# Kernel tuning notes

Hardware: AMD Instinct MI355X
Metric: run time of the kernel (lower is better)

The kernel has to match this reference:

```python
import jax, jax.numpy as jnp
import numpy as np


def setup_inputs() -> dict:
    key = jax.random.key(0)
    ks = jax.random.split(key, 10)
    B, N, E = 8, 20000, 320000
    IN, H = 128, 64
    x = jax.random.normal(ks[0], (B, N, IN), dtype=jnp.float32)
    additional_features = jax.random.normal(ks[1], (B, 1), dtype=jnp.float32)
    edge_index = jax.random.randint(ks[2], (2, E), 0, N, dtype=jnp.int32)
    # GCNConv params (weight applied as x @ W, plus bias)
    W1 = jax.random.normal(ks[3], (IN, H), dtype=jnp.float32) / np.sqrt(IN)
    b1 = jnp.zeros((H,), dtype=jnp.float32)
    W2 = jax.random.normal(ks[4], (H, H), dtype=jnp.float32) / np.sqrt(H)
    b2 = jnp.zeros((H,), dtype=jnp.float32)
    # fc: Linear(hidden + 1, 1)
    fc_w = jax.random.normal(ks[5], (H + 1, 1), dtype=jnp.float32) / np.sqrt(H + 1)
    fc_b = jnp.zeros((1,), dtype=jnp.float32)
    return {"x": x, "additional_features": additional_features, "edge_index": edge_index,
            "W1": W1, "b1": b1, "W2": W2, "b2": b2, "fc_w": fc_w, "fc_b": fc_b}


def reference(x, additional_features, edge_index, W1, b1, W2, b2, fc_w, fc_b):
    # x: [B, N, F]; edge_index: [2, E] shared across the batch (as in the torch code)
    B, N, _ = x.shape
    src = edge_index[0]
    dst = edge_index[1]
    # GCN with self-loops: deg = 1 + in-degree, symmetric normalization
    deg = jnp.ones((N,), jnp.float32).at[dst].add(1.0)
    dis = jax.lax.rsqrt(deg)                      # deg^{-1/2}
    enorm = dis[src] * dis[dst]                   # per-edge norm
    self_norm = (dis * dis)[None, :, None]        # self-loop norm = 1/deg

    def gcn(h, W, b):
        hw = jnp.einsum('bnf,fo->bno', h, W)      # linear transform first
        msgs = hw[:, src, :] * enorm[None, :, None]
        agg = jnp.zeros_like(hw).at[:, dst, :].add(msgs)   # scatter-add to dst
        return agg + hw * self_norm + b

    h = jax.nn.relu(gcn(x, W1, b1))
    h = jax.nn.relu(gcn(h, W2, b2))
    pooled = h.mean(axis=1)                       # global_mean_pool (equal-size graphs)
    cat = jnp.concatenate([pooled, additional_features], axis=1)
    return cat @ fc_w + fc_b                      # [B, 1]
```

## Files before the change

kernel.cpp:

```cpp
#include <hip/hip_runtime.h>

#define BLK 256

typedef __attribute__((ext_vector_type(8))) unsigned short ushort8v;
typedef __attribute__((ext_vector_type(4))) unsigned short ushort4v;
typedef __attribute__((ext_vector_type(8))) short short8v;
typedef __attribute__((ext_vector_type(4))) float f32x4;

static __device__ __forceinline__ float bf2f(unsigned short u) {
    return __uint_as_float(((unsigned)u) << 16);
}
static __device__ __forceinline__ unsigned short f2bf(float f) {
    unsigned u = __float_as_uint(f);
    u += 0x7FFF + ((u >> 16) & 1);
    return (unsigned short)(u >> 16);
}

__global__ void k_init(int* __restrict__ cnt, int N,
                       const float* __restrict__ W1, const float* __restrict__ W2,
                       unsigned short* __restrict__ Wt1, unsigned short* __restrict__ Wt2,
                       int IN, int H) {
    int i = blockIdx.x * BLK + threadIdx.x;
    if (i < N) cnt[i] = 0;
    if (i < IN * H) {
        int k = i / H, c = i % H;
        Wt1[(size_t)c * IN + k] = f2bf(W1[i]);
    }
    if (i < H * H) {
        int k = i / H, c = i % H;
        Wt2[(size_t)c * H + k] = f2bf(W2[i]);
    }
}

__global__ void k_count(const int* __restrict__ dst, int* __restrict__ cnt, int E) {
    int i = blockIdx.x * BLK + threadIdx.x;
    if (i < E) atomicAdd(&cnt[dst[i]], 1);
}

__global__ __launch_bounds__(1024) void k_scan_all(const int* __restrict__ cnt,
                                                   int* __restrict__ rs,
                                                   int* __restrict__ cur, int N) {
    __shared__ int sm[1024];
    const int t = threadIdx.x;
    const int chunk = (N + 1023) >> 10;
    const int lo = t * chunk;
    const int hi = min(lo + chunk, N);
    int s = 0;
    for (int i = lo; i < hi; ++i) s += cnt[i];
    sm[t] = s;
    __syncthreads();
    for (int off = 1; off < 1024; off <<= 1) {
        int v = (t >= off) ? sm[t - off] : 0;
        __syncthreads();
        sm[t] += v;
        __syncthreads();
    }
    int run = sm[t] - s;
    for (int i = lo; i < hi; ++i) {
        int c = cnt[i];
        rs[i] = run; cur[i] = run;
        run += c;
    }
}

__global__ void k_fill(const int* __restrict__ src, const int* __restrict__ dst,
                       const int* __restrict__ cnt, int* __restrict__ cur,
                       int* __restrict__ csrc, float* __restrict__ cw, int E) {
    int e = blockIdx.x * BLK + threadIdx.x;
    if (e >= E) return;
    int d = dst[e], s = src[e];
    int p = atomicAdd(&cur[d], 1);
    csrc[p] = s;
    cw[p] = rsqrtf((1.0f + (float)cnt[s]) * (1.0f + (float)cnt[d]));
}

template <int K>
__global__ __launch_bounds__(BLK) void k_gemm_mfma(const float* __restrict__ A,
                                                   const unsigned short* __restrict__ Wt,
                                                   unsigned short* __restrict__ C,
                                                   int M, int N, int B) {
    constexpr int LDA = K + 8;
    __shared__ unsigned short As[128 * LDA];
    __shared__ unsigned short Bs[64 * LDA];
    const int t = threadIdx.x;
    const int row0 = blockIdx.x * 128;

    for (int i = t; i < 64 * (K / 8); i += BLK) {
        int r = i / (K / 8), c = i % (K / 8);
        *reinterpret_cast<ushort8v*>(&Bs[r * LDA + c * 8]) =
            *reinterpret_cast<const ushort8v*>(Wt + (size_t)r * K + c * 8);
    }
    for (int i = t; i < 128 * (K / 4); i += BLK) {
        int r = i / (K / 4), c = i % (K / 4);
        int gr = row0 + r;
        float4 v = make_float4(0.f, 0.f, 0.f, 0.f);
        if (gr < M) {
            size_t ra = (size_t)(gr % B) * N + (gr / B);
            v = *reinterpret_cast<const float4*>(A + ra * K + c * 4);
        }
        ushort4v o;
        o[0] = f2bf(v.x); o[1] = f2bf(v.y); o[2] = f2bf(v.z); o[3] = f2bf(v.w);
        *reinterpret_cast<ushort4v*>(&As[r * LDA + c * 4]) = o;
    }
    __syncthreads();

    const int w = t >> 6, lane = t & 63;
    const int lrow = lane & 15;
    const int lk = (lane >> 4) * 8;

    f32x4 acc[2][4] = {};
    #pragma unroll
    for (int ks = 0; ks < K / 32; ++ks) {
        short8v a[2], b[4];
        #pragma unroll
        for (int fr = 0; fr < 2; ++fr)
            a[fr] = *reinterpret_cast<const short8v*>(
                &As[(w * 32 + fr * 16 + lrow) * LDA + ks * 32 + lk]);
        #pragma unroll
        for (int fc = 0; fc < 4; ++fc)
            b[fc] = *reinterpret_cast<const short8v*>(
                &Bs[(fc * 16 + lrow) * LDA + ks * 32 + lk]);
        #pragma unroll
        for (int fr = 0; fr < 2; ++fr)
            #pragma unroll
            for (int fc = 0; fc < 4; ++fc)
                acc[fr][fc] = __builtin_amdgcn_mfma_f32_16x16x32_bf16(
                    a[fr], b[fc], acc[fr][fc], 0, 0, 0);
    }

    __syncthreads();
    #pragma unroll
    for (int fr = 0; fr < 2; ++fr)
        #pragma unroll
        for (int fc = 0; fc < 4; ++fc)
            #pragma unroll
            for (int j = 0; j < 4; ++j)
                As[(w * 32 + fr * 16 + (lane >> 4) * 4 + j) * 72 + fc * 16 + lrow] =
                    f2bf(acc[fr][fc][j]);
    __syncthreads();
    for (int i = t; i < 128 * 8; i += BLK) {
        int r = i >> 3, c = i & 7;
        int gr = row0 + r;
        if (gr < M)
            *reinterpret_cast<ushort8v*>(C + (size_t)gr * 64 + c * 8) =
                *reinterpret_cast<const ushort8v*>(&As[r * 72 + c * 8]);
    }
}

#define EDGE_ACC(S, W)                                                              \
    {                                                                               \
        ushort8v _x = *reinterpret_cast<const ushort8v*>(                           \
            hw + (size_t)(S) * 512 + lane * 8);                                     \
        _Pragma("unroll")                                                           \
        for (int j = 0; j < 8; ++j) a[j] = fmaf((W), bf2f(_x[j]), a[j]);            \
    }

__global__ __launch_bounds__(BLK) void k_gather_gemm(const unsigned short* __restrict__ hw,
                                                     const int* __restrict__ rs,
                                                     const int* __restrict__ cnt,
                                                     const int* __restrict__ csrc,
                                                     const float* __restrict__ cw,
                                                     const float* __restrict__ bias,
                                                     const unsigned short* __restrict__ Wt2,
                                                     unsigned short* __restrict__ hw2,
                                                     int N) {
    __shared__ unsigned short Ws[64 * 72];
    __shared__ unsigned short Tile[32 * 72];
    const int t = threadIdx.x;
    const int wv = t >> 6, lane = t & 63;
    const int n = blockIdx.x * 4 + wv;

    for (int i = t; i < 64 * 8; i += BLK) {
        int r = i >> 3, c = i & 7;
        *reinterpret_cast<ushort8v*>(&Ws[r * 72 + c * 8]) =
            *reinterpret_cast<const ushort8v*>(Wt2 + (size_t)r * 64 + c * 8);
    }

    float a[8];
    {
        const int beg = rs[n];
        const int deg = cnt[n];
        const float self = 1.0f / (1.0f + (float)deg);
        const float* bp = bias + (lane & 7) * 8;
        ushort8v v = *reinterpret_cast<const ushort8v*>(hw + (size_t)n * 512 + lane * 8);
        #pragma unroll
        for (int j = 0; j < 8; ++j) a[j] = fmaf(bf2f(v[j]), self, bp[j]);

        int i = 0;
        for (; i + 4 <= deg; i += 4) {
            int s0 = csrc[beg + i],     s1 = csrc[beg + i + 1];
            int s2 = csrc[beg + i + 2], s3 = csrc[beg + i + 3];
            float w0 = cw[beg + i],     w1 = cw[beg + i + 1];
            float w2 = cw[beg + i + 2], w3 = cw[beg + i + 3];
            EDGE_ACC(s0, w0); EDGE_ACC(s1, w1); EDGE_ACC(s2, w2); EDGE_ACC(s3, w3);
        }
        for (; i < deg; ++i) {
            int s0 = csrc[beg + i];
            float w0 = cw[beg + i];
            EDGE_ACC(s0, w0);
        }
    }
    {
        ushort8v o;
        #pragma unroll
        for (int j = 0; j < 8; ++j) o[j] = f2bf(fmaxf(a[j], 0.f));
        *reinterpret_cast<ushort8v*>(&Tile[(wv * 8 + (lane >> 3)) * 72 + (lane & 7) * 8]) = o;
    }
    __syncthreads();

    const int lrow = lane & 15, lk = (lane >> 4) * 8;
    const int r0 = (wv >> 1) * 16, c0 = (wv & 1) * 32;
    f32x4 acc[2] = {};
    #pragma unroll
    for (int ks = 0; ks < 2; ++ks) {
        short8v af = *reinterpret_cast<const short8v*>(&Tile[(r0 + lrow) * 72 + ks * 32 + lk]);
        #pragma unroll
        for (int fc = 0; fc < 2; ++fc) {
            short8v bf_ = *reinterpret_cast<const short8v*>(
                &Ws[(c0 + fc * 16 + lrow) * 72 + ks * 32 + lk]);
            acc[fc] = __builtin_amdgcn_mfma_f32_16x16x32_bf16(af, bf_, acc[fc], 0, 0, 0);
        }
    }
    __syncthreads();
    #pragma unroll
    for (int fc = 0; fc < 2; ++fc)
        #pragma unroll
        for (int j = 0; j < 4; ++j)
            Tile[(r0 + (lane >> 4) * 4 + j) * 72 + c0 + fc * 16 + lrow] = f2bf(acc[fc][j]);
    __syncthreads();
    {
        int r = t >> 3, c = t & 7;
        *reinterpret_cast<ushort8v*>(
            hw2 + (size_t)(blockIdx.x * 4 + (r >> 3)) * 512 + (r & 7) * 64 + c * 8) =
            *reinterpret_cast<const ushort8v*>(&Tile[r * 72 + c * 8]);
    }
}

__global__ __launch_bounds__(BLK) void k_gather_final(const unsigned short* __restrict__ hw,
                                                      const int* __restrict__ rs,
                                                      const int* __restrict__ cnt,
                                                      const int* __restrict__ csrc,
                                                      const float* __restrict__ cw,
                                                      const float* __restrict__ bias,
                                                      const float* __restrict__ fcw,
                                                      float* __restrict__ partial, int N) {
    const int w = threadIdx.x >> 6, lane = threadIdx.x & 63;
    const int n = blockIdx.x * 4 + w;
    float a[8];
    {
        const int beg = rs[n];
        const int deg = cnt[n];
        const float self = 1.0f / (1.0f + (float)deg);
        const float* bp = bias + (lane & 7) * 8;
        ushort8v v = *reinterpret_cast<const ushort8v*>(hw + (size_t)n * 512 + lane * 8);
        #pragma unroll
        for (int j = 0; j < 8; ++j) a[j] = fmaf(bf2f(v[j]), self, bp[j]);

        int i = 0;
        for (; i + 4 <= deg; i += 4) {
            int s0 = csrc[beg + i],     s1 = csrc[beg + i + 1];
            int s2 = csrc[beg + i + 2], s3 = csrc[beg + i + 3];
            float w0 = cw[beg + i],     w1 = cw[beg + i + 1];
            float w2 = cw[beg + i + 2], w3 = cw[beg + i + 3];
            EDGE_ACC(s0, w0); EDGE_ACC(s1, w1); EDGE_ACC(s2, w2); EDGE_ACC(s3, w3);
        }
        for (; i < deg; ++i) {
            int s0 = csrc[beg + i];
            float w0 = cw[beg + i];
            EDGE_ACC(s0, w0);
        }
    }
    __shared__ float sm[4][8];
    const float* fp = fcw + (lane & 7) * 8;
    float s = 0.f;
    #pragma unroll
    for (int j = 0; j < 8; ++j) s = fmaf(fmaxf(a[j], 0.f), fp[j], s);
    #pragma unroll
    for (int off = 1; off < 8; off <<= 1) s += __shfl_xor(s, off, 64);
    if ((lane & 7) == 0) sm[w][lane >> 3] = s;
    __syncthreads();
    if (threadIdx.x < 8)
        partial[(size_t)blockIdx.x * 8 + threadIdx.x] =
            sm[0][threadIdx.x] + sm[1][threadIdx.x] + sm[2][threadIdx.x] + sm[3][threadIdx.x];
}

__global__ void k_finish(const float* __restrict__ partial, int nblk,
                         const float* __restrict__ addf, const float* __restrict__ fcw,
                         const float* __restrict__ fcb, float* __restrict__ out,
                         int N, int H) {
    int b = blockIdx.x;
    float s = 0.f;
    for (int i = threadIdx.x; i < nblk; i += BLK) s += partial[(size_t)i * 8 + b];
    __shared__ float sm[BLK / 64];
    int lane = threadIdx.x & 63, w = threadIdx.x >> 6;
    #pragma unroll
    for (int off = 32; off; off >>= 1) s += __shfl_down(s, off, 64);
    if (lane == 0) sm[w] = s;
    __syncthreads();
    if (threadIdx.x == 0) {
        float t = sm[0] + sm[1] + sm[2] + sm[3];
        out[b] = t / (float)N + addf[b] * fcw[H] + fcb[0];
    }
}

extern "C" void kernel_launch(void* const* d_in, const int* in_sizes, int n_in,
                              void* d_out, int out_size, void* d_ws, size_t ws_size,
                              hipStream_t stream) {
    const float* x    = (const float*)d_in[0];
    const float* addf = (const float*)d_in[1];
    const int*   ei   = (const int*)d_in[2];
    const float* W1   = (const float*)d_in[3];
    const float* b1   = (const float*)d_in[4];
    const float* W2   = (const float*)d_in[5];
    const float* b2   = (const float*)d_in[6];
    const float* fcw  = (const float*)d_in[7];
    const float* fcb  = (const float*)d_in[8];
    float* out = (float*)d_out;

    const int B  = in_sizes[1];
    const int H  = in_sizes[4];
    const int IN = in_sizes[3] / H;
    const int E  = in_sizes[2] / 2;
    const int N  = in_sizes[0] / (B * IN);
    const int* src = ei;
    const int* dst = ei + E;

    const int M = B * N;

    size_t bufsz = (size_t)M * H;
    unsigned short* bufA = (unsigned short*)d_ws;
    unsigned short* bufB = bufA + bufsz;
    int*   cnt   = (int*)(bufB + bufsz);
    int*   rs    = cnt + N;
    int*   cur   = rs + N;
    int*   csrc  = cur + N;
    float* cw    = (float*)(csrc + E);
    unsigned short* Wt1 = (unsigned short*)(cw + E);
    unsigned short* Wt2 = Wt1 + (size_t)H * IN;
    float* partial = (float*)(Wt2 + (size_t)H * H);

    const int nbN = (N + BLK - 1) / BLK;
    const int nbE = (E + BLK - 1) / BLK;
    const int nodes4 = (N + 3) / 4;

    k_init<<<dim3(nbN), dim3(BLK), 0, stream>>>(cnt, N, W1, W2, Wt1, Wt2, IN, H);
    k_count<<<dim3(nbE), dim3(BLK), 0, stream>>>(dst, cnt, E);
    k_scan_all<<<dim3(1), dim3(1024), 0, stream>>>(cnt, rs, cur, N);
    k_fill<<<dim3(nbE), dim3(BLK), 0, stream>>>(src, dst, cnt, cur, csrc, cw, E);

    k_gemm_mfma<128><<<dim3((M + 127) / 128), dim3(BLK), 0, stream>>>(
        x, Wt1, bufA, M, N, B);

    k_gather_gemm<<<dim3(nodes4), dim3(BLK), 0, stream>>>(
        bufA, rs, cnt, csrc, cw, b1, Wt2, bufB, N);

    k_gather_final<<<dim3(nodes4), dim3(BLK), 0, stream>>>(
        bufB, rs, cnt, csrc, cw, b2, fcw, partial, N);

    k_finish<<<dim3(B), dim3(BLK), 0, stream>>>(partial, nodes4, addf, fcw, fcb, out, N, H);
}
```

Measured before the change: 314.4 us.

## Fuse CSR build into cooperative kernel, split node gathers across two waves

The four CSR-building launches are merged into one cooperative kernel that uses grid syncs, with a fallback to the old multi-launch path if the cooperative launch fails. The weight transpose/convert now happens inside each GEMM block instead of in a separate init kernel. Each node's edge gather is split across two wavefronts that take interleaved edges and combine through shared memory, which doubles the waves per node to expose more memory parallelism. The separate final reduction kernel is replaced by atomics plus a last-block-done counter. This trades fewer launches and more latency hiding for redundant per-block weight conversion, a single-block scan inside the cooperative grid, and float atomics with nondeterministic ordering.

Result: slower. 886.5 us (+182.0%).

```diff
diff --git a/kernel.cpp b/kernel.cpp
--- a/kernel.cpp
+++ b/kernel.cpp
@@ -1,4 +1,7 @@
 #include <hip/hip_runtime.h>
+#include <hip/hip_cooperative_groups.h>
+
+namespace cg = cooperative_groups;
 
 #define BLK 256
 
@@ -16,35 +19,75 @@
     return (unsigned short)(u >> 16);
 }
 
-__global__ void k_init(int* __restrict__ cnt, int N,
-                       const float* __restrict__ W1, const float* __restrict__ W2,
-                       unsigned short* __restrict__ Wt1, unsigned short* __restrict__ Wt2,
-                       int IN, int H) {
+__global__ __launch_bounds__(BLK) void k_csr(int* __restrict__ cnt, int* __restrict__ rs,
+                                             int* __restrict__ cur, int* __restrict__ csrc,
+                                             float* __restrict__ cw,
+                                             const int* __restrict__ src,
+                                             const int* __restrict__ dst,
+                                             float* __restrict__ acc, int* __restrict__ ctr,
+                                             int N, int E) {
+    cg::grid_group grid = cg::this_grid();
+    const int t = threadIdx.x;
+    const int gid = blockIdx.x * BLK + t;
+    const int gsz = gridDim.x * BLK;
+
+    for (int i = gid; i < N; i += gsz) cnt[i] = 0;
+    if (gid < 8) acc[gid] = 0.f;
+    if (gid == 8) *ctr = 0;
+    grid.sync();
+
+    for (int i = gid; i < E; i += gsz) atomicAdd(&cnt[dst[i]], 1);
+    grid.sync();
+
+    if (blockIdx.x == 0) {
+        __shared__ int sm[BLK];
+        const int chunk = (N + BLK - 1) / BLK;
+        const int lo = t * chunk, hi = min(lo + chunk, N);
+        int s = 0;
+        for (int i = lo; i < hi; ++i) s += cnt[i];
+        sm[t] = s;
+        __syncthreads();
+        for (int off = 1; off < BLK; off <<= 1) {
+            int v = (t >= off) ? sm[t - off] : 0;
+            __syncthreads();
+            sm[t] += v;
+            __syncthreads();
+        }
+        int run = sm[t] - s;
+        for (int i = lo; i < hi; ++i) {
+            int c = cnt[i];
+            rs[i] = run; cur[i] = run;
+            run += c;
+        }
+    }
+    grid.sync();
+
+    for (int e = gid; e < E; e += gsz) {
+        int d = dst[e], s = src[e];
+        int p = atomicAdd(&cur[d], 1);
+        csrc[p] = s;
+        cw[p] = rsqrtf((1.0f + (float)cnt[s]) * (1.0f + (float)cnt[d]));
+    }
+}
+
+__global__ void k_zero(int* __restrict__ cnt, float* __restrict__ acc,
+                       int* __restrict__ ctr, int N) {
     int i = blockIdx.x * BLK + threadIdx.x;
     if (i < N) cnt[i] = 0;
-    if (i < IN * H) {
-        int k = i / H, c = i % H;
-        Wt1[(size_t)c * IN + k] = f2bf(W1[i]);
-    }
-    if (i < H * H) {
-        int k = i / H, c = i % H;
-        Wt2[(size_t)c * H + k] = f2bf(W2[i]);
-    }
-}
-
+    if (i < 8) acc[i] = 0.f;
+    if (i == 8) *ctr = 0;
+}
 __global__ void k_count(const int* __restrict__ dst, int* __restrict__ cnt, int E) {
     int i = blockIdx.x * BLK + threadIdx.x;
     if (i < E) atomicAdd(&cnt[dst[i]], 1);
 }
-
 __global__ __launch_bounds__(1024) void k_scan_all(const int* __restrict__ cnt,
                                                    int* __restrict__ rs,
                                                    int* __restrict__ cur, int N) {
     __shared__ int sm[1024];
     const int t = threadIdx.x;
     const int chunk = (N + 1023) >> 10;
-    const int lo = t * chunk;
-    const int hi = min(lo + chunk, N);
+    const int lo = t * chunk, hi = min(lo + chunk, N);
     int s = 0;
     for (int i = lo; i < hi; ++i) s += cnt[i];
     sm[t] = s;
@@ -62,7 +105,6 @@
         run += c;
     }
 }
-
 __global__ void k_fill(const int* __restrict__ src, const int* __restrict__ dst,
                        const int* __restrict__ cnt, int* __restrict__ cur,
                        int* __restrict__ csrc, float* __restrict__ cw, int E) {
@@ -76,7 +118,7 @@
 
 template <int K>
 __global__ __launch_bounds__(BLK) void k_gemm_mfma(const float* __restrict__ A,
-                                                   const unsigned short* __restrict__ Wt,
+                                                   const float* __restrict__ W,
                                                    unsigned short* __restrict__ C,
                                                    int M, int N, int B) {
     constexpr int LDA = K + 8;
@@ -85,10 +127,9 @@
     const int t = threadIdx.x;
     const int row0 = blockIdx.x * 128;
 
-    for (int i = t; i < 64 * (K / 8); i += BLK) {
-        int r = i / (K / 8), c = i % (K / 8);
-        *reinterpret_cast<ushort8v*>(&Bs[r * LDA + c * 8]) =
-            *reinterpret_cast<const ushort8v*>(Wt + (size_t)r * K + c * 8);
+    for (int i = t; i < 64 * K; i += BLK) {
+        int k = i >> 6, c = i & 63;
+        Bs[c * LDA + k] = f2bf(W[i]);
     }
     for (int i = t; i < 128 * (K / 4); i += BLK) {
         int r = i / (K / 4), c = i % (K / 4);
@@ -147,12 +188,38 @@
     }
 }
 
-#define EDGE_ACC(S, W)                                                              \
+#define EDGE_ACC(P)                                                                 \
     {                                                                               \
+        int _s = csrc[P];                                                           \
+        float _w = cw[P];                                                           \
         ushort8v _x = *reinterpret_cast<const ushort8v*>(                           \
-            hw + (size_t)(S) * 512 + lane * 8);                                     \
+            hw + (size_t)_s * 512 + lane * 8);                                      \
         _Pragma("unroll")                                                           \
-        for (int j = 0; j < 8; ++j) a[j] = fmaf((W), bf2f(_x[j]), a[j]);            \
+        for (int j = 0; j < 8; ++j) a[j] = fmaf(_w, bf2f(_x[j]), a[j]);             \
+    }
+
+#define GATHER_CORE(NODE)                                                           \
+    float a[8];                                                                     \
+    {                                                                               \
+        const int beg = rs[NODE];                                                   \
+        const int deg = cnt[NODE];                                                  \
+        if (h == 0) {                                                               \
+            const float self = 1.0f / (1.0f + (float)deg);                          \
+            const float* bp = bias + (lane & 7) * 8;                                \
+            ushort8v v = *reinterpret_cast<const ushort8v*>(                        \
+                hw + (size_t)(NODE) * 512 + lane * 8);                              \
+            _Pragma("unroll")                                                       \
+            for (int j = 0; j < 8; ++j) a[j] = fmaf(bf2f(v[j]), self, bp[j]);       \
+        } else {                                                                    \
+            _Pragma("unroll")                                                       \
+            for (int j = 0; j < 8; ++j) a[j] = 0.f;                                 \
+        }                                                                           \
+        int i = beg + h;                                                            \
+        const int end = beg + deg;                                                  \
+        for (; i + 6 < end; i += 8) {                                               \
+            EDGE_ACC(i); EDGE_ACC(i + 2); EDGE_ACC(i + 4); EDGE_ACC(i + 6);         \
+        }                                                                           \
+        for (; i < end; i += 2) EDGE_ACC(i);                                        \
     }
 
 __global__ __launch_bounds__(BLK) void k_gather_gemm(const unsigned short* __restrict__ hw,
@@ -161,77 +228,55 @@
                                                      const int* __restrict__ csrc,
                                                      const float* __restrict__ cw,
                                                      const float* __restrict__ bias,
-                                                     const unsigned short* __restrict__ Wt2,
+                                                     const float* __restrict__ W2,
                                                      unsigned short* __restrict__ hw2,
                                                      int N) {
     __shared__ unsigned short Ws[64 * 72];
-    __shared__ unsigned short Tile[32 * 72];
+    __shared__ unsigned short Tile[16 * 72];
+    __shared__ float comb[2][512];
     const int t = threadIdx.x;
     const int wv = t >> 6, lane = t & 63;
-    const int n = blockIdx.x * 4 + wv;
-
-    for (int i = t; i < 64 * 8; i += BLK) {
-        int r = i >> 3, c = i & 7;
-        *reinterpret_cast<ushort8v*>(&Ws[r * 72 + c * 8]) =
-            *reinterpret_cast<const ushort8v*>(Wt2 + (size_t)r * 64 + c * 8);
-    }
-
-    float a[8];
-    {
-        const int beg = rs[n];
-        const int deg = cnt[n];
-        const float self = 1.0f / (1.0f + (float)deg);
-        const float* bp = bias + (lane & 7) * 8;
-        ushort8v v = *reinterpret_cast<const ushort8v*>(hw + (size_t)n * 512 + lane * 8);
-        #pragma unroll
-        for (int j = 0; j < 8; ++j) a[j] = fmaf(bf2f(v[j]), self, bp[j]);
-
-        int i = 0;
-        for (; i + 4 <= deg; i += 4) {
-            int s0 = csrc[beg + i],     s1 = csrc[beg + i + 1];
-            int s2 = csrc[beg + i + 2], s3 = csrc[beg + i + 3];
-            float w0 = cw[beg + i],     w1 = cw[beg + i + 1];
-            float w2 = cw[beg + i + 2], w3 = cw[beg + i + 3];
-            EDGE_ACC(s0, w0); EDGE_ACC(s1, w1); EDGE_ACC(s2, w2); EDGE_ACC(s3, w3);
-        }
-        for (; i < deg; ++i) {
-            int s0 = csrc[beg + i];
-            float w0 = cw[beg + i];
-            EDGE_ACC(s0, w0);
-        }
-    }
-    {
+    const int s = wv >> 1, h = wv & 1;
+    const int n = blockIdx.x * 2 + s;
+
+    for (int i = t; i < 64 * 64; i += BLK) {
+        int k = i >> 6, c = i & 63;
+        Ws[c * 72 + k] = f2bf(W2[i]);
+    }
+
+    GATHER_CORE(n);
+
+    if (h == 1) {
+        #pragma unroll
+        for (int j = 0; j < 8; ++j) comb[s][j * 64 + lane] = a[j];
+    }
+    __syncthreads();
+    if (h == 0) {
         ushort8v o;
         #pragma unroll
-        for (int j = 0; j < 8; ++j) o[j] = f2bf(fmaxf(a[j], 0.f));
-        *reinterpret_cast<ushort8v*>(&Tile[(wv * 8 + (lane >> 3)) * 72 + (lane & 7) * 8]) = o;
+        for (int j = 0; j < 8; ++j) o[j] = f2bf(fmaxf(a[j] + comb[s][j * 64 + lane], 0.f));
+        *reinterpret_cast<ushort8v*>(&Tile[(s * 8 + (lane >> 3)) * 72 + (lane & 7) * 8]) = o;
     }
     __syncthreads();
 
     const int lrow = lane & 15, lk = (lane >> 4) * 8;
-    const int r0 = (wv >> 1) * 16, c0 = (wv & 1) * 32;
-    f32x4 acc[2] = {};
+    f32x4 acc = {};
     #pragma unroll
     for (int ks = 0; ks < 2; ++ks) {
-        short8v af = *reinterpret_cast<const short8v*>(&Tile[(r0 + lrow) * 72 + ks * 32 + lk]);
-        #pragma unroll
-        for (int fc = 0; fc < 2; ++fc) {
-            short8v bf_ = *reinterpret_cast<const short8v*>(
-                &Ws[(c0 + fc * 16 + lrow) * 72 + ks * 32 + lk]);
-            acc[fc] = __builtin_amdgcn_mfma_f32_16x16x32_bf16(af, bf_, acc[fc], 0, 0, 0);
-        }
+        short8v af = *reinterpret_cast<const short8v*>(&Tile[lrow * 72 + ks * 32 + lk]);
+        short8v bf_ = *reinterpret_cast<const short8v*>(
+            &Ws[(wv * 16 + lrow) * 72 + ks * 32 + lk]);
+        acc = __builtin_amdgcn_mfma_f32_16x16x32_bf16(af, bf_, acc, 0, 0, 0);
     }
     __syncthreads();
     #pragma unroll
-    for (int fc = 0; fc < 2; ++fc)
-        #pragma unroll
-        for (int j = 0; j < 4; ++j)
-            Tile[(r0 + (lane >> 4) * 4 + j) * 72 + c0 + fc * 16 + lrow] = f2bf(acc[fc][j]);
-    __syncthreads();
-    {
+    for (int j = 0; j < 4; ++j)
+        Tile[((lane >> 4) * 4 + j) * 72 + wv * 16 + lrow] = f2bf(acc[j]);
+    __syncthreads();
+    if (t < 128) {
         int r = t >> 3, c = t & 7;
         *reinterpret_cast<ushort8v*>(
-            hw2 + (size_t)(blockIdx.x * 4 + (r >> 3)) * 512 + (r & 7) * 64 + c * 8) =
+            hw2 + (size_t)(blockIdx.x * 2 + (r >> 3)) * 512 + (r & 7) * 64 + c * 8) =
             *reinterpret_cast<const ushort8v*>(&Tile[r * 72 + c * 8]);
     }
 }
@@ -243,63 +288,51 @@
                                                       const float* __restrict__ cw,
                                                       const float* __restrict__ bias,
                                                       const float* __restrict__ fcw,
-                                                      float* __restrict__ partial, int N) {
-    const int w = threadIdx.x >> 6, lane = threadIdx.x & 63;
-    const int n = blockIdx.x * 4 + w;
-    float a[8];
-    {
-        const int beg = rs[n];
-        const int deg = cnt[n];
-        const float self = 1.0f / (1.0f + (float)deg);
-        const float* bp = bias + (lane & 7) * 8;
-        ushort8v v = *reinterpret_cast<const ushort8v*>(hw + (size_t)n * 512 + lane * 8);
-        #pragma unroll
-        for (int j = 0; j < 8; ++j) a[j] = fmaf(bf2f(v[j]), self, bp[j]);
-
-        int i = 0;
-        for (; i + 4 <= deg; i += 4) {
-            int s0 = csrc[beg + i],     s1 = csrc[beg + i + 1];
-            int s2 = csrc[beg + i + 2], s3 = csrc[beg + i + 3];
-            float w0 = cw[beg + i],     w1 = cw[beg + i + 1];
-            float w2 = cw[beg + i + 2], w3 = cw[beg + i + 3];
-            EDGE_ACC(s0, w0); EDGE_ACC(s1, w1); EDGE_ACC(s2, w2); EDGE_ACC(s3, w3);
-        }
-        for (; i < deg; ++i) {
-            int s0 = csrc[beg + i];
-            float w0 = cw[beg + i];
-            EDGE_ACC(s0, w0);
-        }
-    }
-    __shared__ float sm[4][8];
-    const float* fp = fcw + (lane & 7) * 8;
-    float s = 0.f;
-    #pragma unroll
-    for (int j = 0; j < 8; ++j) s = fmaf(fmaxf(a[j], 0.f), fp[j], s);
-    #pragma unroll
-    for (int off = 1; off < 8; off <<= 1) s += __shfl_xor(s, off, 64);
-    if ((lane & 7) == 0) sm[w][lane >> 3] = s;
-    __syncthreads();
-    if (threadIdx.x < 8)
-        partial[(size_t)blockIdx.x * 8 + threadIdx.x] =
-            sm[0][threadIdx.x] + sm[1][threadIdx.x] + sm[2][threadIdx.x] + sm[3][threadIdx.x];
-}
-
-__global__ void k_finish(const float* __restrict__ partial, int nblk,
-                         const float* __restrict__ addf, const float* __restrict__ fcw,
-                         const float* __restrict__ fcb, float* __restrict__ out,
-                         int N, int H) {
-    int b = blockIdx.x;
-    float s = 0.f;
-    for (int i = threadIdx.x; i < nblk; i += BLK) s += partial[(size_t)i * 8 + b];
-    __shared__ float sm[BLK / 64];
-    int lane = threadIdx.x & 63, w = threadIdx.x >> 6;
-    #pragma unroll
-    for (int off = 32; off; off >>= 1) s += __shfl_down(s, off, 64);
-    if (lane == 0) sm[w] = s;
-    __syncthreads();
-    if (threadIdx.x == 0) {
-        float t = sm[0] + sm[1] + sm[2] + sm[3];
-        out[b] = t / (float)N + addf[b] * fcw[H] + fcb[0];
+                                                      const float* __restrict__ addf,
+                                                      const float* __restrict__ fcb,
+                                                      float* __restrict__ acc, int* __restrict__ ctr,
+                                                      float* __restrict__ out,
+                                                      int N, int H, int nblk) {
+    __shared__ float comb[2][512];
+    __shared__ float sm[2][8];
+    __shared__ int lastFlag;
+    const int t = threadIdx.x;
+    const int wv = t >> 6, lane = t & 63;
+    const int s = wv >> 1, h = wv & 1;
+    const int n = blockIdx.x * 2 + s;
+
+    GATHER_CORE(n);
+
+    if (h == 1) {
+        #pragma unroll
+        for (int j = 0; j < 8; ++j) comb[s][j * 64 + lane] = a[j];
+    }
+    __syncthreads();
+    if (h == 0) {
+        const float* fp = fcw + (lane & 7) * 8;
+        float sd = 0.f;
+        #pragma unroll
+        for (int j = 0; j < 8; ++j)
+            sd = fmaf(fmaxf(a[j] + comb[s][j * 64 + lane], 0.f), fp[j], sd);
+        sd += __shfl_xor(sd, 1, 64);
+        sd += __shfl_xor(sd, 2, 64);
+        sd += __shfl_xor(sd, 4, 64);
+        if ((lane & 7) == 0) sm[s][lane >> 3] = sd;
+    }
+    __syncthreads();
+    if (t < 8) {
+        atomicAdd(&acc[t], sm[0][t] + sm[1][t]);
+        __threadfence();
+    }
+    __syncthreads();
+    if (t == 0) {
+        int old = atomicAdd(ctr, 1);
+        lastFlag = (old == nblk - 1) ? 1 : 0;
+    }
+    __syncthreads();
+    if (lastFlag && t < 8) {
+        float v = atomicAdd(&acc[t], 0.f);
+        out[t] = v / (float)N + addf[t] * fcw[H] + fcb[0];
     }
 }
 
@@ -322,40 +355,47 @@
     const int IN = in_sizes[3] / H;
     const int E  = in_sizes[2] / 2;
     const int N  = in_sizes[0] / (B * IN);
-    const int* src = ei;
-    const int* dst = ei + E;
+    const int* srcp = ei;
+    const int* dstp = ei + E;
 
     const int M = B * N;
 
     size_t bufsz = (size_t)M * H;
     unsigned short* bufA = (unsigned short*)d_ws;
     unsigned short* bufB = bufA + bufsz;
-    int*   cnt   = (int*)(bufB + bufsz);
-    int*   rs    = cnt + N;
-    int*   cur   = rs + N;
-    int*   csrc  = cur + N;
-    float* cw    = (float*)(csrc + E);
-    unsigned short* Wt1 = (unsigned short*)(cw + E);
-    unsigned short* Wt2 = Wt1 + (size_t)H * IN;
-    float* partial = (float*)(Wt2 + (size_t)H * H);
+    int*   cnt  = (int*)(bufB + bufsz);
+    int*   rs   = cnt + N;
+    int*   cur  = rs + N;
+    int*   csrc = cur + N;
+    float* cw   = (float*)(csrc + E);
+    float* acc  = (float*)(cw + E);
+    int*   ctr  = (int*)(acc + 8);
 
     const int nbN = (N + BLK - 1) / BLK;
     const int nbE = (E + BLK - 1) / BLK;
-    const int nodes4 = (N + 3) / 4;
-
-    k_init<<<dim3(nbN), dim3(BLK), 0, stream>>>(cnt, N, W1, W2, Wt1, Wt2, IN, H);
-    k_count<<<dim3(nbE), dim3(BLK), 0, stream>>>(dst, cnt, E);
-    k_scan_all<<<dim3(1), dim3(1024), 0, stream>>>(cnt, rs, cur, N);
-    k_fill<<<dim3(nbE), dim3(BLK), 0, stream>>>(src, dst, cnt, cur, csrc, cw, E);
+    const int nodes2 = N / 2;
+
+    {
+        void* args[] = {(void*)&cnt, (void*)&rs, (void*)&cur, (void*)&csrc, (void*)&cw,
+                        (void*)&srcp, (void*)&dstp, (void*)&acc, (void*)&ctr,
+                        (void*)&N, (void*)&E};
+        hipError_t err = hipLaunchCooperativeKernel((const void*)k_csr, dim3(1024),
+                                                    dim3(BLK), args, 0, stream);
+        if (err != hipSuccess) {
+            (void)hipGetLastError();
+            k_zero<<<dim3(nbN), dim3(BLK), 0, stream>>>(cnt, acc, ctr, N);
+            k_count<<<dim3(nbE), dim3(BLK), 0, stream>>>(dstp, cnt, E);
+            k_scan_all<<<dim3(1), dim3(1024), 0, stream>>>(cnt, rs, cur, N);
+            k_fill<<<dim3(nbE), dim3(BLK), 0, stream>>>(srcp, dstp, cnt, cur, csrc, cw, E);
+        }
+    }
 
     k_gemm_mfma<128><<<dim3((M + 127) / 128), dim3(BLK), 0, stream>>>(
-        x, Wt1, bufA, M, N, B);
-
-    k_gather_gemm<<<dim3(nodes4), dim3(BLK), 0, stream>>>(
-        bufA, rs, cnt, csrc, cw, b1, Wt2, bufB, N);
-
-    k_gather_final<<<dim3(nodes4), dim3(BLK), 0, stream>>>(
-        bufB, rs, cnt, csrc, cw, b2, fcw, partial, N);
-
-    k_finish<<<dim3(B), dim3(BLK), 0, stream>>>(partial, nodes4, addf, fcw, fcb, out, N, H);
-}
+        x, W1, bufA, M, N, B);
+
+    k_gather_gemm<<<dim3(nodes2), dim3(BLK), 0, stream>>>(
+        bufA, rs, cnt, csrc, cw, b1, W2, bufB, N);
+
+    k_gather_final<<<dim3(nodes2), dim3(BLK), 0, stream>>>(
+        bufB, rs, cnt, csrc, cw, b2, fcw, addf, fcb, acc, ctr, out, N, H, nodes2);
+}
```
